# Optimization experiments

Hardware: AMD Instinct MI355X
Metric: run time of the kernel (lower is better)

Reference implementation:

```python
import jax, jax.numpy as jnp
import numpy as np

N_SIGMA = 1
K_INST = 8  # instance ids 1..K_INST (0 = background)
W_INST, W_VAR, W_SEED = 1.0, 10.0, 1.0
FG_WEIGHT = 1.0


def make_xym(h, w):
    # torch buffer: linspace(0,2,2048) x / linspace(0,1,1024) y, sliced to [0:h,0:w]
    xm = jnp.linspace(0.0, 2.0, 2048)[:w]
    ym = jnp.linspace(0.0, 1.0, 1024)[:h]
    return jnp.stack([jnp.broadcast_to(xm[None, :], (h, w)),
                      jnp.broadcast_to(ym[:, None], (h, w))], axis=0)  # [2,h,w]


def lovasz_hinge_flat(logits, labels):
    # logits, labels: [N] float (labels in {0,1})
    signs = 2.0 * labels - 1.0
    errors = 1.0 - logits * signs
    order = jnp.argsort(-errors)            # descending sort of errors
    errors_sorted = errors[order]
    gt_sorted = labels[order]
    gts = gt_sorted.sum()
    inter = gts - jnp.cumsum(gt_sorted)
    union = gts + jnp.cumsum(1.0 - gt_sorted)
    jac = 1.0 - inter / union
    grad = jnp.concatenate([jac[:1], jac[1:] - jac[:-1]])
    # torch impl wraps grad in Variable() -> no gradient through grad
    return jnp.dot(jax.nn.relu(errors_sorted), jax.lax.stop_gradient(grad))


def spatial_emb_loss(predictions, instances):
    B, C, T, h, w = predictions.shape
    xym = make_xym(h, w)
    # Faithful to the torch source: due to loop indentation, only the last
    # time step's var/instance/seed losses survive, and obj_count == 1.
    pred = predictions[:, :, T - 1]          # [B,C,h,w]
    inst = instances[:, 0, T - 1]            # [B,h,w] int
    spatial_emb = jnp.tanh(pred[:, 0:2]) + xym[None]   # [B,2,h,w]
    sigma = pred[:, 2:2 + N_SIGMA]                     # [B,1,h,w]
    seed = jax.nn.sigmoid(pred[:, 2 + N_SIGMA])        # [B,h,w]
    npix = float(h * w)

    def per_image(se, sig, sd, ins):
        bg_loss = jnp.sum(jnp.where(ins == 0, sd ** 2, 0.0))

        def per_id(k):
            m = (ins == k).astype(se.dtype)            # [h,w]
            cnt = m.sum()
            safe = jnp.maximum(cnt, 1.0)
            # to_center=True: center of in-mask pixel coordinates
            center = jnp.sum(xym * m[None], axis=(1, 2)) / safe      # [2]
            s_mean = jnp.sum(sig * m[None], axis=(1, 2)) / safe      # [n_sigma]
            var_l = jnp.sum(m[None] * (sig - jax.lax.stop_gradient(s_mean)[:, None, None]) ** 2) / (safe * N_SIGMA)
            s_exp = jnp.exp(s_mean * 10.0)
            dist = jnp.exp(-jnp.sum((se - center[:, None, None]) ** 2 * s_exp[:, None, None], axis=0))  # [h,w]
            inst_l = lovasz_hinge_flat((dist * 2.0 - 1.0).reshape(-1), m.reshape(-1))
            seed_l = FG_WEIGHT * jnp.sum(m * (sd - jax.lax.stop_gradient(dist)) ** 2)
            present = (cnt > 0).astype(se.dtype)       # torch skips absent ids
            return present * var_l, present * inst_l, present * seed_l

        var_l, inst_l, seed_l = jax.vmap(per_id)(jnp.arange(1, K_INST + 1))
        seed_loss = (bg_loss + seed_l.sum()) / npix
        # obj_count == 1 in the original code (incremented once per t-loop)
        return W_INST * inst_l.sum() + W_VAR * var_l.sum() + W_SEED * seed_loss

    per_b = jax.vmap(per_image)(spatial_emb, sigma, seed, inst)
    # torch: loss = loss / b, with b == B-1 after the loop
    return per_b.sum() / (B - 1)


def setup_inputs():
    key = jax.random.key(0)
    k1, k2 = jax.random.split(key)
    B, C, T, H, W = 4, 4, 2, 512, 1024
    predictions = jax.random.normal(k1, (B, C, T, H, W), dtype=jnp.float32)
    instances = jax.random.randint(k2, (B, 1, T, H, W), 0, K_INST + 1, dtype=jnp.int32)
    labels = jnp.zeros((B, 1, T, H, W), dtype=jnp.int32)  # unused by forward
    return {"predictions": predictions, "instances": instances, "labels": labels}


def reference(predictions, instances, labels):
    return spatial_emb_loss(predictions, instances)
```

## Files before the change

kernel.cpp:

```cpp
#include <hip/hip_runtime.h>

#define H 512
#define WID 1024
#define HW (H*WID)
#define B 4
#define K 8
#define NB 1024
#define NBLK1 128

#define OFF_LOSS  0
#define OFF_FIN   16
#define OFF_SPART 512
#define OFF_RED   (OFF_SPART + B*K*NBLK1*5)
#define OFF_PART  (OFF_RED + 2*B*K*NB)

static __device__ __forceinline__ float frcp(float x){
#if __has_builtin(__builtin_amdgcn_rcpf)
  return __builtin_amdgcn_rcpf(x);
#else
  return 1.0f / x;
#endif
}
static __device__ __forceinline__ float fexp2(float x){
#if __has_builtin(__builtin_amdgcn_exp2f)
  return __builtin_amdgcn_exp2f(x);
#else
  return exp2f(x);
#endif
}
static __device__ __forceinline__ float ftanh(float x){
  return 1.0f - 2.0f * frcp(__expf(2.0f*x) + 1.0f);
}
static __device__ __forceinline__ float fsigmoid(float x){
  return frcp(1.0f + __expf(-x));
}

__global__ __launch_bounds__(512) void k1_stats(const float* __restrict__ pred,
                                                const int* __restrict__ inst,
                                                float* __restrict__ ws) {
  const int b = blockIdx.y;
  __shared__ int4   ti[1024];
  __shared__ float4 ts[1024];
  __shared__ float  part5[K][5];
  const float4* sig4 = (const float4*)(pred + (size_t)(8*b + 5) * HW);
  const int4*   ins4 = (const int4*)(inst + (size_t)(2*b + 1) * HW);
  const int base4 = blockIdx.x * 1024;
  #pragma unroll
  for (int i = 0; i < 2; i++) {
    const int q = threadIdx.x + i*512;
    ti[q] = ins4[base4 + q];
    ts[q] = sig4[base4 + q];
  }
  __syncthreads();
  const int wv = threadIdx.x >> 6, lane = threadIdx.x & 63;
  const int kk = wv + 1;
  float cnt=0.f, sx=0.f, sy=0.f, ss=0.f, ss2=0.f;
  #pragma unroll
  for (int j = 0; j < 16; j++) {
    const int q = lane + 64*j;
    const int4   iv = ti[q];
    const float4 sv = ts[q];
    const int p = (base4 + q) * 4;
    const float xm0 = (float)(p & (WID-1)) * (2.0f/2047.0f);
    const float ym  = (float)(p >> 10)     * (1.0f/1023.0f);
    const float m0 = (iv.x==kk)?1.f:0.f, m1=(iv.y==kk)?1.f:0.f,
                m2 = (iv.z==kk)?1.f:0.f, m3=(iv.w==kk)?1.f:0.f;
    const float msum = (m0+m1)+(m2+m3);
    cnt += msum;
    sx  += msum*xm0 + (m1 + 2.0f*m2 + 3.0f*m3)*(2.0f/2047.0f);
    sy  += msum*ym;
    ss  += m0*sv.x + m1*sv.y + m2*sv.z + m3*sv.w;
    ss2 += m0*sv.x*sv.x + m1*sv.y*sv.y + m2*sv.z*sv.z + m3*sv.w*sv.w;
  }
  #pragma unroll
  for (int o=1;o<64;o<<=1){
    cnt+=__shfl_xor(cnt,o,64);
    sx +=__shfl_xor(sx, o,64);
    sy +=__shfl_xor(sy, o,64);
    ss +=__shfl_xor(ss, o,64);
    ss2+=__shfl_xor(ss2,o,64);
  }
  if (lane == 0) {
    part5[wv][0]=cnt; part5[wv][1]=sx; part5[wv][2]=sy; part5[wv][3]=ss; part5[wv][4]=ss2;
  }
  __syncthreads();
  if (threadIdx.x < K*5) {
    const int w = threadIdx.x / 5, c = threadIdx.x % 5;
    ws[OFF_SPART + ((size_t)(b*K + w)*NBLK1 + blockIdx.x)*5 + c] = part5[w][c];
  }
}

__global__ __launch_bounds__(256) void k2_fin(float* __restrict__ ws) {
  const int t = threadIdx.x;
  const int bk = t >> 3, s = t & 7;
  float a0=0.f,a1=0.f,a2=0.f,a3=0.f,a4=0.f;
  for (int j = 0; j < NBLK1/8; j++) {
    const float* p = ws + OFF_SPART + ((size_t)bk*NBLK1 + (s + 8*j))*5;
    a0+=p[0]; a1+=p[1]; a2+=p[2]; a3+=p[3]; a4+=p[4];
  }
  #pragma unroll
  for (int o=1;o<8;o<<=1){
    a0+=__shfl_xor(a0,o,64); a1+=__shfl_xor(a1,o,64); a2+=__shfl_xor(a2,o,64);
    a3+=__shfl_xor(a3,o,64); a4+=__shfl_xor(a4,o,64);
  }
  __shared__ float vloc[32];
  if (s == 0) {
    const float cnt=a0, sx=a1, sy=a2, ss=a3, ss2=a4;
    const float present = (cnt > 0.0f) ? 1.0f : 0.0f;
    const float safe = fmaxf(cnt, 1.0f);
    const float cx = sx/safe, cy = sy/safe, sm = ss/safe;
    const float var = (ss2 - 2.0f*sm*ss + sm*sm*cnt)/safe;
    const float sexp = expf(10.0f * sm);
    const float L2E = 1.4426950408889634f;
    float* fin = ws + OFF_FIN + bk*8;
    fin[0] = -sexp*L2E;
    fin[1] =  2.0f*sexp*cx*L2E;
    fin[2] =  2.0f*sexp*cy*L2E;
    fin[3] = -sexp*(cx*cx + cy*cy)*L2E + 10.0f;
    fin[4] = cnt;
    vloc[bk] = present * 10.0f * var * (1.0f/3.0f);
  }
  __syncthreads();
  if (t == 0) {
    float v = 0.f;
    #pragma unroll
    for (int i = 0; i < 32; i++) v += vloc[i];
    atomicAdd(ws + OFF_LOSS, v);
  }
}

template<int G>
__global__ __launch_bounds__(256) void k3_main(const float* __restrict__ pred,
                                               const int* __restrict__ inst,
                                               float* __restrict__ ws,
                                               unsigned int* __restrict__ part) {
  const int b = blockIdx.y, g = blockIdx.x;
  __shared__ unsigned int hist[K*NB];
  for (int i = threadIdx.x; i < K*NB; i += 256) hist[i] = 0;
  float4 fr[K];
  #pragma unroll
  for (int k=0;k<K;k++){
    const float* fin = ws + OFF_FIN + (b*K + k)*8;
    fr[k] = make_float4(fin[0], fin[1], fin[2], fin[3]);
  }
  __syncthreads();
  const float4* p0 = (const float4*)(pred + (size_t)(8*b+1)*HW);
  const float4* p1 = (const float4*)(pred + (size_t)(8*b+3)*HW);
  const float4* p3 = (const float4*)(pred + (size_t)(8*b+7)*HW);
  const int4*   in4 = (const int4*)(inst + (size_t)(2*b+1)*HW);
  float sAcc = 0.0f;
  constexpr int CH4 = HW / (G*4);
  const int base4 = g * CH4;
  #pragma unroll
  for (int q0 = 0; q0 < CH4; q0 += 256) {
    const int idx = base4 + q0 + threadIdx.x;
    const int4   iv = in4[idx];
    const float4 f0 = p0[idx];
    const float4 f1 = p1[idx];
    const float4 f3 = p3[idx];
    const int p = idx * 4;
    const float xm0 = (float)(p & (WID-1)) * (2.0f/2047.0f);
    const float ym  = (float)(p >> 10)     * (1.0f/1023.0f);
    const int   ivv[4] = {iv.x, iv.y, iv.z, iv.w};
    const float a0v[4] = {f0.x, f0.y, f0.z, f0.w};
    const float a1v[4] = {f1.x, f1.y, f1.z, f1.w};
    const float a3v[4] = {f3.x, f3.y, f3.z, f3.w};
    #pragma unroll
    for (int e4 = 0; e4 < 4; e4++) {
      const int ivp = ivv[e4];
      const float px = ftanh(a0v[e4]) + xm0 + (float)e4*(2.0f/2047.0f);
      const float py = ftanh(a1v[e4]) + ym;
      const float sd = fsigmoid(a3v[e4]);
      const float t2 = px*px + py*py;
      float down = 0.0f;
      #pragma unroll
      for (int j=0;j<K;j++){
        const float u = fmaf(fr[j].x, t2, fmaf(fr[j].y, px, fmaf(fr[j].z, py, fr[j].w)));
        const float v = fexp2(u);
        int vi = (int)v; vi = (vi > NB-1) ? NB-1 : vi;
        const bool own = (ivp == j+1);
        const int bu = own ? (NB-1 - vi) : vi;
        if (own) down = v;
        atomicAdd(&hist[j*NB + bu], own ? 0x10001u : 1u);
      }
      const float d  = (ivp == 0) ? 0.0f : down * (1.0f/1024.0f);
      const float df = sd - d;
      sAcc += df*df;
    }
  }
  __syncthreads();
  unsigned int* dst = part + ((size_t)b*G + g)*(K*NB);
  for (int i = threadIdx.x; i < K*NB; i += 256) dst[i] = hist[i];
  #pragma unroll
  for (int o=1;o<64;o<<=1) sAcc += __shfl_xor(sAcc, o, 64);
  __shared__ float wsum[4];
  if ((threadIdx.x & 63) == 0) wsum[threadIdx.x>>6] = sAcc;
  __syncthreads();
  if (threadIdx.x == 0) {
    const float tot = wsum[0]+wsum[1]+wsum[2]+wsum[3];
    atomicAdd(ws + OFF_LOSS, tot * (1.0f/((float)HW * 3.0f)));
  }
}

__global__ __launch_bounds__(128) void k4a_reduce(const unsigned int* __restrict__ part,
                                                  unsigned int* __restrict__ red, int G) {
  const int bk = blockIdx.x, c = blockIdx.y;
  const int b = bk >> 3, k = bk & 7;
  const int bu = c*128 + threadIdx.x;
  const unsigned int* base = part + (size_t)b*G*K*NB + (size_t)k*NB + bu;
  unsigned int rc = 0, rp = 0;
  #pragma unroll 4
  for (int g = 0; g < G; g++) {
    const unsigned int v = base[(size_t)g*K*NB];
    rc += v & 0xFFFFu;
    rp += v >> 16;
  }
  red[bk*NB + bu]            = rc;
  red[B*K*NB + bk*NB + bu]   = rp;
}

__global__ __launch_bounds__(256) void k4b_lovasz(const unsigned int* __restrict__ red,
                                                   float* __restrict__ ws) {
  const int bk = blockIdx.x;
  const float cntF = ws[OFF_FIN + bk*8 + 4];
  if (cntF <= 0.0f) return;
  const double Pd = (double)cntF;
  const int t = threadIdx.x;
  const int lane = t & 63, wv = t >> 6;
  unsigned int cnt[4], pos[4];
  #pragma unroll
  for (int j = 0; j < 4; j++) {
    const int bu = NB-1 - (t*4 + j);
    cnt[j] = red[bk*NB + bu];
    pos[j] = red[B*K*NB + bk*NB + bu];
  }
  const int lc = (int)(cnt[0]+cnt[1]+cnt[2]+cnt[3]);
  const int lp = (int)(pos[0]+pos[1]+pos[2]+pos[3]);
  int ic = lc, ip = lp;
  #pragma unroll
  for (int o=1;o<64;o<<=1){
    const int vc = __shfl_up(ic, o, 64);
    const int vp = __shfl_up(ip, o, 64);
    if (lane >= o) { ic += vc; ip += vp; }
  }
  __shared__ int wtc[4], wtp[4];
  if (lane == 63) { wtc[wv] = ic; wtp[wv] = ip; }
  __syncthreads();
  int offc = 0, offp = 0;
  for (int w = 0; w < wv; w++) { offc += wtc[w]; offp += wtp[w]; }
  int irun = offc + ic - lc;
  int crun = offp + ip - lp;
  double acc = 0.0;
  #pragma unroll
  for (int j = 0; j < 4; j++) {
    const int n = (int)cnt[j];
    if (n) {
      const int bu = NB-1 - (t*4 + j);
      const double jac0 = (irun==0) ? 0.0 : 1.0 - (Pd - crun)/(Pd + irun - crun);
      irun += n; crun += (int)pos[j];
      const double jac1 = 1.0 - (Pd - crun)/(Pd + irun - crun);
      acc += ((bu + 0.5) * (2.0/NB)) * (jac1 - jac0);
    }
  }
  #pragma unroll
  for (int o=1;o<64;o<<=1) acc += __shfl_xor(acc, o, 64);
  __shared__ double racc[4];
  if (lane == 0) racc[wv] = acc;
  __syncthreads();
  if (t == 0) {
    const double tot = racc[0]+racc[1]+racc[2]+racc[3];
    atomicAdd(ws + OFF_LOSS, (float)(tot * (1.0/3.0)));
  }
}

__global__ void k5_out(const float* __restrict__ ws, float* __restrict__ out) {
  if (threadIdx.x == 0) out[0] = ws[OFF_LOSS];
}

extern "C" void kernel_launch(void* const* d_in, const int* in_sizes, int n_in,
                              void* d_out, int out_size, void* d_ws, size_t ws_size,
                              hipStream_t stream) {
  const float* pred = (const float*)d_in[0];
  const int*   inst = (const int*)d_in[1];
  float* ws  = (float*)d_ws;
  float* out = (float*)d_out;
  unsigned int* red  = ((unsigned int*)d_ws) + OFF_RED;
  unsigned int* part = ((unsigned int*)d_ws) + OFF_PART;
  int G = 128;
  while (G > 32 && ws_size < ((size_t)OFF_PART + (size_t)B*G*K*NB)*4) G >>= 1;
  hipMemsetAsync(d_ws, 0, (size_t)OFF_FIN*4 + 64, stream);
  k1_stats<<<dim3(NBLK1,B), 512, 0, stream>>>(pred, inst, ws);
  k2_fin  <<<1, 256, 0, stream>>>(ws);
  if      (G == 128) k3_main<128><<<dim3(128,B), 256, 0, stream>>>(pred, inst, ws, part);
  else if (G ==  64) k3_main< 64><<<dim3( 64,B), 256, 0, stream>>>(pred, inst, ws, part);
  else               k3_main< 32><<<dim3( 32,B), 256, 0, stream>>>(pred, inst, ws, part);
  k4a_reduce<<<dim3(B*K, 8), 128, 0, stream>>>(part, red, G);
  k4b_lovasz<<<B*K, 256, 0, stream>>>(red, ws);
  k5_out  <<<1, 64, 0, stream>>>(ws, out);
}
```

Baseline: 142.0 us.

## Double k3 grid, interleave per-element histogram updates, and merge adjacent atomics

The main histogram kernel now loops over instance ids outermost and the four vector elements innermost. Equal bucket indices among adjacent elements are merged into a single LDS atomic. The launch uses 256 blocks per image instead of 128 when workspace allows, with a launch-bounds occupancy hint and a deeper unroll in the reduction. This targets LDS atomic contention and low occupancy, at the cost of a larger partial-histogram buffer and more reduction work in k4a.

```diff
diff --git a/kernel.cpp b/kernel.cpp
--- a/kernel.cpp
+++ b/kernel.cpp
@@ -130,10 +130,10 @@
 }
 
 template<int G>
-__global__ __launch_bounds__(256) void k3_main(const float* __restrict__ pred,
-                                               const int* __restrict__ inst,
-                                               float* __restrict__ ws,
-                                               unsigned int* __restrict__ part) {
+__global__ __launch_bounds__(256, 4) void k3_main(const float* __restrict__ pred,
+                                                  const int* __restrict__ inst,
+                                                  float* __restrict__ ws,
+                                                  unsigned int* __restrict__ part) {
   const int b = blockIdx.y, g = blockIdx.x;
   __shared__ unsigned int hist[K*NB];
   for (int i = threadIdx.x; i < K*NB; i += 256) hist[i] = 0;
@@ -161,31 +161,51 @@
     const int p = idx * 4;
     const float xm0 = (float)(p & (WID-1)) * (2.0f/2047.0f);
     const float ym  = (float)(p >> 10)     * (1.0f/1023.0f);
-    const int   ivv[4] = {iv.x, iv.y, iv.z, iv.w};
-    const float a0v[4] = {f0.x, f0.y, f0.z, f0.w};
-    const float a1v[4] = {f1.x, f1.y, f1.z, f1.w};
-    const float a3v[4] = {f3.x, f3.y, f3.z, f3.w};
+    const int ivv[4] = {iv.x, iv.y, iv.z, iv.w};
+    float pxv[4], pyv[4], t2v[4], down[4];
+    {
+      const float a0v[4] = {f0.x, f0.y, f0.z, f0.w};
+      const float a1v[4] = {f1.x, f1.y, f1.z, f1.w};
+      #pragma unroll
+      for (int e=0;e<4;e++){
+        pxv[e] = ftanh(a0v[e]) + xm0 + (float)e*(2.0f/2047.0f);
+        pyv[e] = ftanh(a1v[e]) + ym;
+        t2v[e] = pxv[e]*pxv[e] + pyv[e]*pyv[e];
+        down[e] = 0.0f;
+      }
+    }
     #pragma unroll
-    for (int e4 = 0; e4 < 4; e4++) {
-      const int ivp = ivv[e4];
-      const float px = ftanh(a0v[e4]) + xm0 + (float)e4*(2.0f/2047.0f);
-      const float py = ftanh(a1v[e4]) + ym;
-      const float sd = fsigmoid(a3v[e4]);
-      const float t2 = px*px + py*py;
-      float down = 0.0f;
+    for (int j=0;j<K;j++){
+      const float4 f = fr[j];
+      int buv[4]; unsigned addv[4];
       #pragma unroll
-      for (int j=0;j<K;j++){
-        const float u = fmaf(fr[j].x, t2, fmaf(fr[j].y, px, fmaf(fr[j].z, py, fr[j].w)));
+      for (int e=0;e<4;e++){
+        const float u = fmaf(f.x, t2v[e], fmaf(f.y, pxv[e], fmaf(f.z, pyv[e], f.w)));
         const float v = fexp2(u);
         int vi = (int)v; vi = (vi > NB-1) ? NB-1 : vi;
-        const bool own = (ivp == j+1);
-        const int bu = own ? (NB-1 - vi) : vi;
-        if (own) down = v;
-        atomicAdd(&hist[j*NB + bu], own ? 0x10001u : 1u);
+        const bool own = (ivv[e] == j+1);
+        if (own) down[e] = v;
+        buv[e] = own ? (NB-1 - vi) : vi;
+        addv[e] = own ? 0x10001u : 1u;
       }
-      const float d  = (ivp == 0) ? 0.0f : down * (1.0f/1024.0f);
-      const float df = sd - d;
-      sAcc += df*df;
+      int cur = buv[0]; unsigned acc = addv[0];
+      #pragma unroll
+      for (int e=1;e<4;e++){
+        const bool same = (buv[e] == cur);
+        if (!same) atomicAdd(&hist[j*NB + cur], acc);
+        acc = same ? acc + addv[e] : addv[e];
+        cur = buv[e];
+      }
+      atomicAdd(&hist[j*NB + cur], acc);
+    }
+    {
+      const float sdv[4] = {fsigmoid(f3.x), fsigmoid(f3.y), fsigmoid(f3.z), fsigmoid(f3.w)};
+      #pragma unroll
+      for (int e=0;e<4;e++){
+        const float d  = (ivv[e] == 0) ? 0.0f : down[e] * (1.0f/1024.0f);
+        const float df = sdv[e] - d;
+        sAcc += df*df;
+      }
     }
   }
   __syncthreads();
@@ -209,7 +229,7 @@
   const int bu = c*128 + threadIdx.x;
   const unsigned int* base = part + (size_t)b*G*K*NB + (size_t)k*NB + bu;
   unsigned int rc = 0, rp = 0;
-  #pragma unroll 4
+  #pragma unroll 8
   for (int g = 0; g < G; g++) {
     const unsigned int v = base[(size_t)g*K*NB];
     rc += v & 0xFFFFu;
@@ -286,12 +306,13 @@
   float* out = (float*)d_out;
   unsigned int* red  = ((unsigned int*)d_ws) + OFF_RED;
   unsigned int* part = ((unsigned int*)d_ws) + OFF_PART;
-  int G = 128;
+  int G = 256;
   while (G > 32 && ws_size < ((size_t)OFF_PART + (size_t)B*G*K*NB)*4) G >>= 1;
   hipMemsetAsync(d_ws, 0, (size_t)OFF_FIN*4 + 64, stream);
   k1_stats<<<dim3(NBLK1,B), 512, 0, stream>>>(pred, inst, ws);
   k2_fin  <<<1, 256, 0, stream>>>(ws);
-  if      (G == 128) k3_main<128><<<dim3(128,B), 256, 0, stream>>>(pred, inst, ws, part);
+  if      (G == 256) k3_main<256><<<dim3(256,B), 256, 0, stream>>>(pred, inst, ws, part);
+  else if (G == 128) k3_main<128><<<dim3(128,B), 256, 0, stream>>>(pred, inst, ws, part);
   else if (G ==  64) k3_main< 64><<<dim3( 64,B), 256, 0, stream>>>(pred, inst, ws, part);
   else               k3_main< 32><<<dim3( 32,B), 256, 0, stream>>>(pred, inst, ws, part);
   k4a_reduce<<<dim3(B*K, 8), 128, 0, stream>>>(part, red, G);
```

Result: slower. 149.1 us (+5.0%).
